# Kernel tuning notes

Measured on AMD Instinct MI355X. Metric: run time of the kernel, lower is better.

## Reference

```python
import jax, jax.numpy as jnp
import numpy as np

S, B, H = 512, 64, 1024


def setup_inputs() -> dict:
    key = jax.random.key(0)
    ks = jax.random.split(key, 9)
    sc = 1.0 / np.sqrt(2 * H)
    return {
        "hidden": jax.random.normal(ks[0], (B, H), jnp.float32),
        "decoder_out": jax.random.normal(ks[1], (B, H), jnp.float32),
        "encoder_states": jax.random.normal(ks[2], (S, B, H), jnp.float32),
        "W_attn": jax.random.uniform(ks[3], (2 * H, 2 * H), jnp.float32, -sc, sc),
        "b_attn": jax.random.uniform(ks[4], (2 * H,), jnp.float32, -sc, sc),
        "W_attn2": jax.random.uniform(ks[5], (1, 2 * H), jnp.float32, -sc, sc),
        "b_attn2": jax.random.uniform(ks[6], (1,), jnp.float32, -sc, sc),
        "W_comb": jax.random.uniform(ks[7], (H, 2 * H), jnp.float32, -sc, sc),
        "b_comb": jax.random.uniform(ks[8], (H,), jnp.float32, -sc, sc),
    }


def reference(hidden, decoder_out, encoder_states, W_attn, b_attn, W_attn2, b_attn2, W_comb, b_comb):
    s, b, h = encoder_states.shape
    # per-timestep cat(hidden, enc_t) -> attn -> tanh -> attn2, fully batched over S
    hid = jnp.broadcast_to(hidden[None], (s, b, h))
    cat = jnp.concatenate([hid, encoder_states], axis=-1)            # [S,B,2H]
    scores = jnp.tanh(cat @ W_attn.T + b_attn) @ W_attn2.T + b_attn2  # [S,B,1]
    scores = scores[..., 0].T                                         # [B,S] (stack dim=1 + squeeze)
    attn_w = jax.nn.softmax(scores, axis=-1)                          # [B,S]
    # bmm([B,1,S], [B,S,H]) -> [B,H]
    applied = jnp.einsum("bs,sbh->bh", attn_w, encoder_states)
    out = jnp.concatenate([decoder_out, applied], axis=-1) @ W_comb.T + b_comb
    out = jnp.tanh(out)
    return out, applied
```

## Files before the change

kernel.cpp:

```cpp
#include <hip/hip_runtime.h>
#include <stdint.h>


typedef __attribute__((ext_vector_type(8))) short bf16x8;
typedef __attribute__((ext_vector_type(4))) float f32x4;

__device__ __forceinline__ float bf2f(uint16_t u) {
  return __uint_as_float(((uint32_t)u) << 16);
}
__device__ __forceinline__ uint16_t f2bf(float x) {
  uint32_t u = __float_as_uint(x);
  u += 0x7fffu + ((u >> 16) & 1u);
  return (uint16_t)(u >> 16);
}
__device__ __forceinline__ uint32_t pk2(float a, float b) {
  return (uint32_t)f2bf(a) | ((uint32_t)f2bf(b) << 16);
}
__device__ __forceinline__ uint4 cvt8(const float* __restrict__ p) {
  const float4 a = *(const float4*)p;
  const float4 b = *(const float4*)(p + 4);
  uint4 r;
  r.x = pk2(a.x, a.y); r.y = pk2(a.z, a.w);
  r.z = pk2(b.x, b.y); r.w = pk2(b.z, b.w);
  return r;
}
__device__ __forceinline__ float tanh_fast(float x) {
  const float e = __expf(2.f * x);
  return __builtin_fmaf(-2.f, __builtin_amdgcn_rcpf(e + 1.f), 1.f);
}
__device__ __forceinline__ void load16(const uint16_t* g, uint16_t* l) {
  __builtin_amdgcn_global_load_lds(
      (const __attribute__((address_space(1))) void*)g,
      (__attribute__((address_space(3))) void*)l, 16, 0, 0);
}

__global__ __launch_bounds__(256)
void cvt_all_kernel(const float* __restrict__ enc, const float* __restrict__ Wa,
                    const float* __restrict__ Wc,
                    uint16_t* __restrict__ enc_bf, uint16_t* __restrict__ Wa_bf,
                    uint16_t* __restrict__ Wc_bf,
                    float* __restrict__ scores, float* __restrict__ U,
                    const float* __restrict__ ba) {
  const int tid0 = blockIdx.x * 256 + threadIdx.x;
  if (tid0 < 32768) {
    scores[tid0] = 0.f;
#pragma unroll
    for (int k = 0; k < 4; ++k) {
      const int i = tid0 * 4 + k;
      U[i] = ba[i & 2047];
    }
  }
  const int stride = gridDim.x * 256;
  for (int idx = tid0; idx < 4718592; idx += stride) {
    if (idx < 4194304) {
      ((uint4*)enc_bf)[idx] = cvt8(enc + (size_t)idx * 8);
    } else if (idx < 4456448) {
      const int k = idx - 4194304;
      const int j = k >> 7, c8 = k & 127;
      ((uint4*)Wa_bf)[k] = cvt8(Wa + (size_t)j * 2048 + 1024 + c8 * 8);
    } else {
      const int k = idx - 4456448;
      ((uint4*)Wc_bf)[k] = cvt8(Wc + (size_t)k * 8);
    }
  }
}

__global__ __launch_bounds__(256)
void gemm_u_kernel(const float* __restrict__ A, const float* __restrict__ B32,
                   float* __restrict__ U) {
  __shared__ __align__(16) uint16_t sA[128 * 32];
  __shared__ __align__(16) uint16_t sB[128 * 32];
  const int t = threadIdx.x, lane = t & 63, wave = t >> 6;
  const int wm = wave >> 1, wn = wave & 1;
  const int bn0 = blockIdx.x * 128;
  const int kbase = blockIdx.y * 256;
  const int srow = t >> 2, scol = (t & 3) * 8;
  const int ar0 = min(srow, 63), ar1 = min(64 + srow, 63);
  f32x4 acc[4][4];
#pragma unroll
  for (int i = 0; i < 4; ++i)
#pragma unroll
    for (int j = 0; j < 4; ++j) acc[i][j] = (f32x4){0.f, 0.f, 0.f, 0.f};
  const int mrow = wm * 64 + (lane & 15);
  const int nrow = wn * 64 + (lane & 15);
  const int kq = (lane >> 4) * 8;
  for (int kk = 0; kk < 8; ++kk) {
    const int k0 = kbase + (kk << 5);
    const uint4 va0 = cvt8(A + (size_t)ar0 * 1024 + scol + k0);
    const uint4 va1 = cvt8(A + (size_t)ar1 * 1024 + scol + k0);
    const uint4 vb0 = cvt8(B32 + (size_t)(bn0 + srow) * 2048 + scol + k0);
    const uint4 vb1 = cvt8(B32 + (size_t)(bn0 + 64 + srow) * 2048 + scol + k0);
    __syncthreads();
    *(uint4*)&sA[t * 8] = va0;
    *(uint4*)&sA[2048 + t * 8] = va1;
    *(uint4*)&sB[t * 8] = vb0;
    *(uint4*)&sB[2048 + t * 8] = vb1;
    __syncthreads();
    bf16x8 af[4], bfr[4];
#pragma unroll
    for (int i = 0; i < 4; ++i) af[i] = *(const bf16x8*)&sA[(mrow + i * 16) * 32 + kq];
#pragma unroll
    for (int j = 0; j < 4; ++j) bfr[j] = *(const bf16x8*)&sB[(nrow + j * 16) * 32 + kq];
#pragma unroll
    for (int i = 0; i < 4; ++i)
#pragma unroll
      for (int j = 0; j < 4; ++j)
        acc[i][j] = __builtin_amdgcn_mfma_f32_16x16x32_bf16(af[i], bfr[j], acc[i][j], 0, 0, 0);
  }
  const int colb = lane & 15, rquad = lane >> 4;
#pragma unroll
  for (int i = 0; i < 4; ++i)
#pragma unroll
    for (int r = 0; r < 4; ++r) {
      const int gm = wm * 64 + i * 16 + rquad * 4 + r;
      if (gm < 64) {
#pragma unroll
        for (int j = 0; j < 4; ++j) {
          const int gn = bn0 + wn * 64 + j * 16 + colb;
          atomicAdd(&U[gm * 2048 + gn], acc[i][j][r]);
        }
      }
    }
}

__global__ __launch_bounds__(512, 4)
void gemm_score_kernel(const uint16_t* __restrict__ A,
                       const uint16_t* __restrict__ Bm,
                       float* __restrict__ outf,
                       const float* __restrict__ Ubias,
                       const float* __restrict__ bias) {
  __shared__ __align__(16) uint16_t lds[2][12288];

  const int t = threadIdx.x, lane = t & 63, wave = t >> 6;
  const int wm = wave >> 2, wn = wave & 3;
  const int wid = blockIdx.x;
  const int xcd = wid & 7, q = wid >> 3;
  const int bm0 = (xcd * 32 + (q >> 3)) * 128;
  const int bn0 = (q & 7) * 256;

  const int rA = t >> 2, kcA = t & 3;
  const uint16_t* gpA =
      A + (size_t)(bm0 + rA) * 1024 + (kcA ^ ((rA >> 1) & 3)) * 8;
  const uint16_t* gpB[2];
#pragma unroll
  for (int qq = 0; qq < 2; ++qq) {
    const int sl = qq * 512 + t;
    const int r = sl >> 2, kc = sl & 3;
    gpB[qq] = Bm + (size_t)(bn0 + r) * 1024 + (kc ^ ((r >> 1) & 3)) * 8;
  }
  const int sbA = wave * 512;
  const int sbB0 = 4096 + wave * 512;
  const int sbB1 = 4096 + 4096 + wave * 512;

  f32x4 acc[4][4];
#pragma unroll
  for (int i = 0; i < 4; ++i)
#pragma unroll
    for (int j = 0; j < 4; ++j) acc[i][j] = (f32x4){0.f, 0.f, 0.f, 0.f};

  const int swz = ((lane >> 1) & 3) << 3;
  const int kq = ((lane >> 4) * 8) ^ swz;
  const int rl = lane & 15;
  const int aoff = (wm * 64 + rl) * 32 + kq;
  const int boff = (wn * 64 + rl) * 32 + kq;

  load16(gpA, &lds[0][sbA]);
  load16(gpB[0], &lds[0][sbB0]);
  load16(gpB[1], &lds[0][sbB1]);
  __syncthreads();

#pragma unroll
  for (int s = 0; s < 32; ++s) {
    const int cb = s & 1;
    if (s + 1 < 32) {
      const int nb = cb ^ 1, ko = (s + 1) * 32;
      load16(gpA + ko, &lds[nb][sbA]);
      load16(gpB[0] + ko, &lds[nb][sbB0]);
      load16(gpB[1] + ko, &lds[nb][sbB1]);
    }
    const uint16_t* sA = &lds[cb][0];
    const uint16_t* sB = &lds[cb][4096];
    bf16x8 af[4], bfr[4];
#pragma unroll
    for (int i = 0; i < 4; ++i) af[i] = *(const bf16x8*)&sA[aoff + i * 512];
#pragma unroll
    for (int j = 0; j < 4; ++j) bfr[j] = *(const bf16x8*)&sB[boff + j * 512];
#pragma unroll
    for (int i = 0; i < 4; ++i)
#pragma unroll
      for (int j = 0; j < 4; ++j)
        acc[i][j] = __builtin_amdgcn_mfma_f32_16x16x32_bf16(af[i], bfr[j], acc[i][j], 0, 0, 0);
    __syncthreads();
  }

  const int colb = lane & 15, rquad = lane >> 4;
  float w2f[4];
#pragma unroll
  for (int j = 0; j < 4; ++j) w2f[j] = bias[bn0 + wn * 64 + j * 16 + colb];
#pragma unroll
  for (int i = 0; i < 4; ++i) {
#pragma unroll
    for (int r = 0; r < 4; ++r) {
      const int gm = bm0 + wm * 64 + i * 16 + rquad * 4 + r;
      const int bb = gm & 63;
      float p = 0.f;
#pragma unroll
      for (int j = 0; j < 4; ++j) {
        const float u = Ubias[bb * 2048 + bn0 + wn * 64 + j * 16 + colb];
        p += tanh_fast(acc[i][j][r] + u) * w2f[j];
      }
      p += __shfl_xor(p, 1);
      p += __shfl_xor(p, 2);
      p += __shfl_xor(p, 4);
      p += __shfl_xor(p, 8);
      if (colb == 0) atomicAdd(outf + gm, p);
    }
  }
}

__global__ __launch_bounds__(512)
void gemm_comb_kernel(const uint16_t* __restrict__ A,
                      const uint16_t* __restrict__ Bm,
                      float* __restrict__ outp,
                      const float* __restrict__ bias) {
  const int t = threadIdx.x, lane = t & 63, wave = t >> 6;
  const int g = blockIdx.x * 8 + wave;
  const int m0 = (g >> 6) * 16, n0 = (g & 63) * 16;
  const int rl = lane & 15, kq = (lane >> 4) * 8;
  const uint16_t* ap = A + (size_t)(m0 + rl) * 2048 + kq;
  const uint16_t* bp = Bm + (size_t)(n0 + rl) * 2048 + kq;
  f32x4 acc = (f32x4){0.f, 0.f, 0.f, 0.f};
#pragma unroll 8
  for (int ks = 0; ks < 64; ++ks) {
    const bf16x8 af = *(const bf16x8*)(ap + ks * 32);
    const bf16x8 bf = *(const bf16x8*)(bp + ks * 32);
    acc = __builtin_amdgcn_mfma_f32_16x16x32_bf16(af, bf, acc, 0, 0, 0);
  }
  const int gm = m0 + (lane >> 4) * 4;
  const int gn = n0 + rl;
  const float bj = bias[gn];
#pragma unroll
  for (int r = 0; r < 4; ++r)
    outp[(gm + r) * 1024 + gn] = tanh_fast(acc[r] + bj);
}

__global__ __launch_bounds__(256)
void applied_kernel(const uint16_t* __restrict__ encb, const float* __restrict__ dec,
                    const float* __restrict__ scores,
                    float* __restrict__ out_applied, uint16_t* __restrict__ acat) {
  const int b = blockIdx.x, chunk = blockIdx.y, t = threadIdx.x;
  const int wave = t >> 6, lane = t & 63;
  __shared__ float w[512];
  __shared__ float red[8];
  __shared__ float2 part2[256];
  float v0 = scores[(size_t)t * 64 + b];
  float v1 = scores[(size_t)(t + 256) * 64 + b];
  float mx = fmaxf(v0, v1);
#pragma unroll
  for (int off = 32; off >= 1; off >>= 1) mx = fmaxf(mx, __shfl_xor(mx, off));
  if (lane == 0) red[wave] = mx;
  __syncthreads();
  mx = fmaxf(fmaxf(red[0], red[1]), fmaxf(red[2], red[3]));
  const float e0 = __expf(v0 - mx), e1 = __expf(v1 - mx);
  float sum = e0 + e1;
#pragma unroll
  for (int off = 32; off >= 1; off >>= 1) sum += __shfl_xor(sum, off);
  if (lane == 0) red[4 + wave] = sum;
  __syncthreads();
  sum = (red[4] + red[5]) + (red[6] + red[7]);
  const float inv = 1.f / sum;
  w[t] = e0 * inv;
  w[t + 256] = e1 * inv;
  __syncthreads();
  const int hp = t & 31, sq = t >> 5;
  const int h = chunk * 64 + hp * 2;
  const uint32_t* base = (const uint32_t*)encb + (size_t)b * 512 + (h >> 1);
  float a0 = 0.f, a1 = 0.f;
#pragma unroll 8
  for (int s = sq * 64; s < sq * 64 + 64; ++s) {
    const uint32_t p = base[(size_t)s * 32768];
    a0 += w[s] * bf2f((uint16_t)(p & 0xffffu));
    a1 += w[s] * bf2f((uint16_t)(p >> 16));
  }
  part2[t] = make_float2(a0, a1);
  __syncthreads();
  if (t < 32) {
    a0 = 0.f; a1 = 0.f;
#pragma unroll
    for (int k = 0; k < 8; ++k) {
      const float2 pp = part2[t + 32 * k];
      a0 += pp.x; a1 += pp.y;
    }
    *(float2*)(out_applied + (size_t)b * 1024 + h) = make_float2(a0, a1);
    *(uint32_t*)(acat + (size_t)b * 2048 + 1024 + h) = pk2(a0, a1);
    *(uint32_t*)(acat + (size_t)b * 2048 + h) =
        pk2(dec[(size_t)b * 1024 + h], dec[(size_t)b * 1024 + h + 1]);
  }
}

extern "C" void kernel_launch(void* const* d_in, const int* in_sizes, int n_in,
                              void* d_out, int out_size, void* d_ws, size_t ws_size,
                              hipStream_t stream) {
  const float* hidden  = (const float*)d_in[0];
  const float* dec     = (const float*)d_in[1];
  const float* enc     = (const float*)d_in[2];
  const float* W_attn  = (const float*)d_in[3];
  const float* b_attn  = (const float*)d_in[4];
  const float* W_attn2 = (const float*)d_in[5];
  const float* W_comb  = (const float*)d_in[7];
  const float* b_comb  = (const float*)d_in[8];
  float* outp = (float*)d_out;

  char* ws = (char*)d_ws;
  float*    scores = (float*)(ws + 0);
  float*    U      = (float*)(ws + 131072);
  uint16_t* acat   = (uint16_t*)(ws + 655360);
  uint16_t* enc_bf = (uint16_t*)(ws + 1048576);
  uint16_t* Wa_bf  = (uint16_t*)(ws + 68157440);
  uint16_t* Wc_bf  = (uint16_t*)(ws + 72351744);

  cvt_all_kernel<<<4608, 256, 0, stream>>>(enc, W_attn, W_comb, enc_bf, Wa_bf,
                                           Wc_bf, scores, U, b_attn);
  gemm_u_kernel<<<dim3(16, 4), 256, 0, stream>>>(hidden, W_attn, U);
  gemm_score_kernel<<<2048, 512, 0, stream>>>(enc_bf, Wa_bf, scores, U, W_attn2);
  applied_kernel<<<dim3(64, 16), 256, 0, stream>>>(enc_bf, dec, scores,
                                                   outp + 65536, acat);
  gemm_comb_kernel<<<32, 512, 0, stream>>>(acat, Wc_bf, outp, b_comb);
}
```

Baseline: 467.4 us.

## Fuse fp32-to-bf16 encoder conversion into score GEMM with triple-buffered pipeline

Removes the separate pass that converts the 128MB fp32 encoder tensor to bf16. The score GEMM now loads fp32 encoder rows into registers, converts them, and writes bf16 to LDS through a three-stage buffer, while the weight tiles still arrive by direct global-to-LDS loads. The M tile grows to 256 rows with occupancy 1, and the applied kernel reads fp32 encoder data directly. Bias init moves into the U GEMM and zeroing moves to a memset. This cuts one full write and read of the converted encoder, at the cost of register pressure, lower occupancy and fp32 reads in the applied kernel.

Result: slower. 537.0 us (+14.9%).

```diff
diff --git a/kernel.cpp b/kernel.cpp
--- a/kernel.cpp
+++ b/kernel.cpp
@@ -35,39 +35,21 @@
 }
 
 __global__ __launch_bounds__(256)
-void cvt_all_kernel(const float* __restrict__ enc, const float* __restrict__ Wa,
-                    const float* __restrict__ Wc,
-                    uint16_t* __restrict__ enc_bf, uint16_t* __restrict__ Wa_bf,
-                    uint16_t* __restrict__ Wc_bf,
-                    float* __restrict__ scores, float* __restrict__ U,
-                    const float* __restrict__ ba) {
-  const int tid0 = blockIdx.x * 256 + threadIdx.x;
-  if (tid0 < 32768) {
-    scores[tid0] = 0.f;
-#pragma unroll
-    for (int k = 0; k < 4; ++k) {
-      const int i = tid0 * 4 + k;
-      U[i] = ba[i & 2047];
-    }
-  }
-  const int stride = gridDim.x * 256;
-  for (int idx = tid0; idx < 4718592; idx += stride) {
-    if (idx < 4194304) {
-      ((uint4*)enc_bf)[idx] = cvt8(enc + (size_t)idx * 8);
-    } else if (idx < 4456448) {
-      const int k = idx - 4194304;
-      const int j = k >> 7, c8 = k & 127;
-      ((uint4*)Wa_bf)[k] = cvt8(Wa + (size_t)j * 2048 + 1024 + c8 * 8);
-    } else {
-      const int k = idx - 4456448;
-      ((uint4*)Wc_bf)[k] = cvt8(Wc + (size_t)k * 8);
-    }
+void cvt_w_kernel(const float* __restrict__ Wa, const float* __restrict__ Wc,
+                  uint16_t* __restrict__ Wa_bf, uint16_t* __restrict__ Wc_bf) {
+  const int idx = blockIdx.x * 256 + threadIdx.x;
+  if (idx < 262144) {
+    const int j = idx >> 7, c8 = idx & 127;
+    ((uint4*)Wa_bf)[idx] = cvt8(Wa + (size_t)j * 2048 + 1024 + c8 * 8);
+  } else {
+    const int k = idx - 262144;
+    ((uint4*)Wc_bf)[k] = cvt8(Wc + (size_t)k * 8);
   }
 }
 
 __global__ __launch_bounds__(256)
 void gemm_u_kernel(const float* __restrict__ A, const float* __restrict__ B32,
-                   float* __restrict__ U) {
+                   float* __restrict__ U, const float* __restrict__ ba) {
   __shared__ __align__(16) uint16_t sA[128 * 32];
   __shared__ __align__(16) uint16_t sB[128 * 32];
   const int t = threadIdx.x, lane = t & 63, wave = t >> 6;
@@ -108,6 +90,7 @@
         acc[i][j] = __builtin_amdgcn_mfma_f32_16x16x32_bf16(af[i], bfr[j], acc[i][j], 0, 0, 0);
   }
   const int colb = lane & 15, rquad = lane >> 4;
+  const float bsc = (blockIdx.y == 0) ? 1.f : 0.f;
 #pragma unroll
   for (int i = 0; i < 4; ++i)
 #pragma unroll
@@ -117,80 +100,123 @@
 #pragma unroll
         for (int j = 0; j < 4; ++j) {
           const int gn = bn0 + wn * 64 + j * 16 + colb;
-          atomicAdd(&U[gm * 2048 + gn], acc[i][j][r]);
+          atomicAdd(&U[gm * 2048 + gn], acc[i][j][r] + bsc * ba[gn]);
         }
       }
     }
 }
 
-__global__ __launch_bounds__(512, 4)
-void gemm_score_kernel(const uint16_t* __restrict__ A,
+__global__ __launch_bounds__(512, 1)
+void gemm_score_kernel(const float* __restrict__ encf,
                        const uint16_t* __restrict__ Bm,
                        float* __restrict__ outf,
                        const float* __restrict__ Ubias,
                        const float* __restrict__ bias) {
-  __shared__ __align__(16) uint16_t lds[2][12288];
+  __shared__ __align__(16) uint16_t lds[3][2][8192];
 
   const int t = threadIdx.x, lane = t & 63, wave = t >> 6;
   const int wm = wave >> 2, wn = wave & 3;
   const int wid = blockIdx.x;
   const int xcd = wid & 7, q = wid >> 3;
-  const int bm0 = (xcd * 32 + (q >> 3)) * 128;
+  const int bm0 = (xcd * 16 + (q >> 3)) * 256;
   const int bn0 = (q & 7) * 256;
 
-  const int rA = t >> 2, kcA = t & 3;
-  const uint16_t* gpA =
-      A + (size_t)(bm0 + rA) * 1024 + (kcA ^ ((rA >> 1) & 3)) * 8;
-  const uint16_t* gpB[2];
+  const float* gA[2];
+  const uint16_t* gB[2];
+  int sb[2];
 #pragma unroll
   for (int qq = 0; qq < 2; ++qq) {
     const int sl = qq * 512 + t;
     const int r = sl >> 2, kc = sl & 3;
-    gpB[qq] = Bm + (size_t)(bn0 + r) * 1024 + (kc ^ ((r >> 1) & 3)) * 8;
-  }
-  const int sbA = wave * 512;
-  const int sbB0 = 4096 + wave * 512;
-  const int sbB1 = 4096 + 4096 + wave * 512;
-
-  f32x4 acc[4][4];
-#pragma unroll
-  for (int i = 0; i < 4; ++i)
+    const int g = kc ^ ((r >> 1) & 3);
+    gA[qq] = encf + (size_t)(bm0 + r) * 1024 + g * 8;
+    gB[qq] = Bm + (size_t)(bn0 + r) * 1024 + g * 8;
+    sb[qq] = (qq * 512 + wave * 64) * 8;
+  }
+  const int wA0 = t * 8;
+  const int wA1 = 4096 + t * 8;
+
+  f32x4 acc[8][4];
+#pragma unroll
+  for (int i = 0; i < 8; ++i)
 #pragma unroll
     for (int j = 0; j < 4; ++j) acc[i][j] = (f32x4){0.f, 0.f, 0.f, 0.f};
 
   const int swz = ((lane >> 1) & 3) << 3;
   const int kq = ((lane >> 4) * 8) ^ swz;
   const int rl = lane & 15;
-  const int aoff = (wm * 64 + rl) * 32 + kq;
+  const int aoff = (wm * 128 + rl) * 32 + kq;
   const int boff = (wn * 64 + rl) * 32 + kq;
 
-  load16(gpA, &lds[0][sbA]);
-  load16(gpB[0], &lds[0][sbB0]);
-  load16(gpB[1], &lds[0][sbB1]);
-  __syncthreads();
-
-#pragma unroll
-  for (int s = 0; s < 32; ++s) {
-    const int cb = s & 1;
-    if (s + 1 < 32) {
-      const int nb = cb ^ 1, ko = (s + 1) * 32;
-      load16(gpA + ko, &lds[nb][sbA]);
-      load16(gpB[0] + ko, &lds[nb][sbB0]);
-      load16(gpB[1] + ko, &lds[nb][sbB1]);
-    }
-    const uint16_t* sA = &lds[cb][0];
-    const uint16_t* sB = &lds[cb][4096];
-    bf16x8 af[4], bfr[4];
-#pragma unroll
-    for (int i = 0; i < 4; ++i) af[i] = *(const bf16x8*)&sA[aoff + i * 512];
+  float4 av[2][2];
+#pragma unroll
+  for (int qq = 0; qq < 2; ++qq) {
+    av[qq][0] = *(const float4*)(gA[qq]);
+    av[qq][1] = *(const float4*)(gA[qq] + 4);
+  }
+#pragma unroll
+  for (int qq = 0; qq < 2; ++qq) load16(gB[qq], &lds[0][1][sb[qq]]);
+#pragma unroll
+  for (int qq = 0; qq < 2; ++qq) load16(gB[qq] + 32, &lds[1][1][sb[qq]]);
+  asm volatile("s_waitcnt vmcnt(2)" ::: "memory");
+  {
+    uint4 w0, w1;
+    w0.x = pk2(av[0][0].x, av[0][0].y); w0.y = pk2(av[0][0].z, av[0][0].w);
+    w0.z = pk2(av[0][1].x, av[0][1].y); w0.w = pk2(av[0][1].z, av[0][1].w);
+    w1.x = pk2(av[1][0].x, av[1][0].y); w1.y = pk2(av[1][0].z, av[1][0].w);
+    w1.z = pk2(av[1][1].x, av[1][1].y); w1.w = pk2(av[1][1].z, av[1][1].w);
+    *(uint4*)&lds[0][0][wA0] = w0;
+    *(uint4*)&lds[0][0][wA1] = w1;
+  }
+  asm volatile("s_waitcnt lgkmcnt(0)" ::: "memory");
+  __builtin_amdgcn_s_barrier();
+
+  constexpr int NT = 32;
+#pragma unroll
+  for (int kt = 0; kt < NT; ++kt) {
+    const int cb = kt % 3;
+    if (kt + 1 < NT) {
+      const int ko = (kt + 1) * 32;
+#pragma unroll
+      for (int qq = 0; qq < 2; ++qq) {
+        av[qq][0] = *(const float4*)(gA[qq] + ko);
+        av[qq][1] = *(const float4*)(gA[qq] + ko + 4);
+      }
+    }
+    if (kt + 2 < NT) {
+      const int nb2 = (kt + 2) % 3, ko2 = (kt + 2) * 32;
+#pragma unroll
+      for (int qq = 0; qq < 2; ++qq) load16(gB[qq] + ko2, &lds[nb2][1][sb[qq]]);
+    }
+    const uint16_t* sA = lds[cb][0];
+    const uint16_t* sB = lds[cb][1];
+    bf16x8 af[8], bfr[4];
+#pragma unroll
+    for (int i = 0; i < 8; ++i) af[i] = *(const bf16x8*)&sA[aoff + i * 512];
 #pragma unroll
     for (int j = 0; j < 4; ++j) bfr[j] = *(const bf16x8*)&sB[boff + j * 512];
 #pragma unroll
-    for (int i = 0; i < 4; ++i)
+    for (int i = 0; i < 8; ++i)
 #pragma unroll
       for (int j = 0; j < 4; ++j)
         acc[i][j] = __builtin_amdgcn_mfma_f32_16x16x32_bf16(af[i], bfr[j], acc[i][j], 0, 0, 0);
-    __syncthreads();
+    if (kt + 1 < NT) {
+      if (kt + 2 < NT) {
+        asm volatile("s_waitcnt vmcnt(2)" ::: "memory");
+      } else {
+        asm volatile("s_waitcnt vmcnt(0)" ::: "memory");
+      }
+      const int nb1 = (kt + 1) % 3;
+      uint4 w0, w1;
+      w0.x = pk2(av[0][0].x, av[0][0].y); w0.y = pk2(av[0][0].z, av[0][0].w);
+      w0.z = pk2(av[0][1].x, av[0][1].y); w0.w = pk2(av[0][1].z, av[0][1].w);
+      w1.x = pk2(av[1][0].x, av[1][0].y); w1.y = pk2(av[1][0].z, av[1][0].w);
+      w1.z = pk2(av[1][1].x, av[1][1].y); w1.w = pk2(av[1][1].z, av[1][1].w);
+      *(uint4*)&lds[nb1][0][wA0] = w0;
+      *(uint4*)&lds[nb1][0][wA1] = w1;
+      asm volatile("s_waitcnt lgkmcnt(0)" ::: "memory");
+      __builtin_amdgcn_s_barrier();
+    }
   }
 
   const int colb = lane & 15, rquad = lane >> 4;
@@ -198,10 +224,10 @@
 #pragma unroll
   for (int j = 0; j < 4; ++j) w2f[j] = bias[bn0 + wn * 64 + j * 16 + colb];
 #pragma unroll
-  for (int i = 0; i < 4; ++i) {
+  for (int i = 0; i < 8; ++i) {
 #pragma unroll
     for (int r = 0; r < 4; ++r) {
-      const int gm = bm0 + wm * 64 + i * 16 + rquad * 4 + r;
+      const int gm = bm0 + wm * 128 + i * 16 + rquad * 4 + r;
       const int bb = gm & 63;
       float p = 0.f;
 #pragma unroll
@@ -245,7 +271,7 @@
 }
 
 __global__ __launch_bounds__(256)
-void applied_kernel(const uint16_t* __restrict__ encb, const float* __restrict__ dec,
+void applied_kernel(const float* __restrict__ encf, const float* __restrict__ dec,
                     const float* __restrict__ scores,
                     float* __restrict__ out_applied, uint16_t* __restrict__ acat) {
   const int b = blockIdx.x, chunk = blockIdx.y, t = threadIdx.x;
@@ -274,13 +300,13 @@
   __syncthreads();
   const int hp = t & 31, sq = t >> 5;
   const int h = chunk * 64 + hp * 2;
-  const uint32_t* base = (const uint32_t*)encb + (size_t)b * 512 + (h >> 1);
+  const float2* base = (const float2*)encf + (((size_t)b * 1024 + h) >> 1);
   float a0 = 0.f, a1 = 0.f;
 #pragma unroll 8
   for (int s = sq * 64; s < sq * 64 + 64; ++s) {
-    const uint32_t p = base[(size_t)s * 32768];
-    a0 += w[s] * bf2f((uint16_t)(p & 0xffffu));
-    a1 += w[s] * bf2f((uint16_t)(p >> 16));
+    const float2 p = base[(size_t)s * 32768];
+    a0 += w[s] * p.x;
+    a1 += w[s] * p.y;
   }
   part2[t] = make_float2(a0, a1);
   __syncthreads();
@@ -315,15 +341,14 @@
   float*    scores = (float*)(ws + 0);
   float*    U      = (float*)(ws + 131072);
   uint16_t* acat   = (uint16_t*)(ws + 655360);
-  uint16_t* enc_bf = (uint16_t*)(ws + 1048576);
   uint16_t* Wa_bf  = (uint16_t*)(ws + 68157440);
   uint16_t* Wc_bf  = (uint16_t*)(ws + 72351744);
 
-  cvt_all_kernel<<<4608, 256, 0, stream>>>(enc, W_attn, W_comb, enc_bf, Wa_bf,
-                                           Wc_bf, scores, U, b_attn);
-  gemm_u_kernel<<<dim3(16, 4), 256, 0, stream>>>(hidden, W_attn, U);
-  gemm_score_kernel<<<2048, 512, 0, stream>>>(enc_bf, Wa_bf, scores, U, W_attn2);
-  applied_kernel<<<dim3(64, 16), 256, 0, stream>>>(enc_bf, dec, scores,
+  hipMemsetAsync(ws, 0, 655360, stream);
+  cvt_w_kernel<<<2048, 256, 0, stream>>>(W_attn, W_comb, Wa_bf, Wc_bf);
+  gemm_u_kernel<<<dim3(16, 4), 256, 0, stream>>>(hidden, W_attn, U, b_attn);
+  gemm_score_kernel<<<1024, 512, 0, stream>>>(enc, Wa_bf, scores, U, W_attn2);
+  applied_kernel<<<dim3(64, 16), 256, 0, stream>>>(enc, dec, scores,
                                                    outp + 65536, acat);
   gemm_comb_kernel<<<32, 512, 0, stream>>>(acat, Wc_bf, outp, b_comb);
 }
```

## Merge U-GEMM into conversion kernel and enlarge score GEMM tile with triple buffering

Applied to the files above, without the earlier changes.

The small hidden·W_attn GEMM now runs as extra blocks of the fp32-to-bf16 conversion kernel, and the bias is folded into its atomic adds, which saves one launch. Scores and U are zeroed by a memset instead. The score GEMM tile grows from 128x256 to 256x256 per block (8x4 MFMA accumulators per wave), and the LDS pipeline goes from double to triple buffering with explicit vmcnt waits. The aim is more operand reuse and better latency hiding, at the cost of higher register pressure (launch bounds drop to 2 blocks) and fewer blocks.

Result: no change. 465.0 us (-0.5%).

```diff
diff --git a/kernel.cpp b/kernel.cpp
--- a/kernel.cpp
+++ b/kernel.cpp
@@ -35,45 +35,37 @@
 }
 
 __global__ __launch_bounds__(256)
-void cvt_all_kernel(const float* __restrict__ enc, const float* __restrict__ Wa,
-                    const float* __restrict__ Wc,
-                    uint16_t* __restrict__ enc_bf, uint16_t* __restrict__ Wa_bf,
-                    uint16_t* __restrict__ Wc_bf,
-                    float* __restrict__ scores, float* __restrict__ U,
-                    const float* __restrict__ ba) {
-  const int tid0 = blockIdx.x * 256 + threadIdx.x;
-  if (tid0 < 32768) {
-    scores[tid0] = 0.f;
-#pragma unroll
-    for (int k = 0; k < 4; ++k) {
-      const int i = tid0 * 4 + k;
-      U[i] = ba[i & 2047];
-    }
-  }
-  const int stride = gridDim.x * 256;
-  for (int idx = tid0; idx < 4718592; idx += stride) {
-    if (idx < 4194304) {
-      ((uint4*)enc_bf)[idx] = cvt8(enc + (size_t)idx * 8);
-    } else if (idx < 4456448) {
-      const int k = idx - 4194304;
-      const int j = k >> 7, c8 = k & 127;
-      ((uint4*)Wa_bf)[k] = cvt8(Wa + (size_t)j * 2048 + 1024 + c8 * 8);
-    } else {
-      const int k = idx - 4456448;
-      ((uint4*)Wc_bf)[k] = cvt8(Wc + (size_t)k * 8);
-    }
-  }
-}
-
-__global__ __launch_bounds__(256)
-void gemm_u_kernel(const float* __restrict__ A, const float* __restrict__ B32,
-                   float* __restrict__ U) {
-  __shared__ __align__(16) uint16_t sA[128 * 32];
-  __shared__ __align__(16) uint16_t sB[128 * 32];
-  const int t = threadIdx.x, lane = t & 63, wave = t >> 6;
+void cvt_gemmu_kernel(const float* __restrict__ enc, const float* __restrict__ Wa,
+                      const float* __restrict__ Wc,
+                      uint16_t* __restrict__ enc_bf, uint16_t* __restrict__ Wa_bf,
+                      uint16_t* __restrict__ Wc_bf,
+                      const float* __restrict__ hidden, float* __restrict__ U,
+                      const float* __restrict__ ba) {
+  __shared__ __align__(16) uint16_t sAB[2][128 * 32];
+  const int t = threadIdx.x;
+  if (blockIdx.x < 4608) {
+    const int stride = 4608 * 256;
+    for (int idx = blockIdx.x * 256 + t; idx < 4718592; idx += stride) {
+      if (idx < 4194304) {
+        ((uint4*)enc_bf)[idx] = cvt8(enc + (size_t)idx * 8);
+      } else if (idx < 4456448) {
+        const int k = idx - 4194304;
+        const int j = k >> 7, c8 = k & 127;
+        ((uint4*)Wa_bf)[k] = cvt8(Wa + (size_t)j * 2048 + 1024 + c8 * 8);
+      } else {
+        const int k = idx - 4456448;
+        ((uint4*)Wc_bf)[k] = cvt8(Wc + (size_t)k * 8);
+      }
+    }
+    return;
+  }
+  const int bx = blockIdx.x - 4608;
+  uint16_t* sA = sAB[0];
+  uint16_t* sB = sAB[1];
+  const int lane = t & 63, wave = t >> 6;
   const int wm = wave >> 1, wn = wave & 1;
-  const int bn0 = blockIdx.x * 128;
-  const int kbase = blockIdx.y * 256;
+  const int bn0 = (bx & 15) * 128;
+  const int kbase = (bx >> 4) * 256;
   const int srow = t >> 2, scol = (t & 3) * 8;
   const int ar0 = min(srow, 63), ar1 = min(64 + srow, 63);
   f32x4 acc[4][4];
@@ -86,10 +78,10 @@
   const int kq = (lane >> 4) * 8;
   for (int kk = 0; kk < 8; ++kk) {
     const int k0 = kbase + (kk << 5);
-    const uint4 va0 = cvt8(A + (size_t)ar0 * 1024 + scol + k0);
-    const uint4 va1 = cvt8(A + (size_t)ar1 * 1024 + scol + k0);
-    const uint4 vb0 = cvt8(B32 + (size_t)(bn0 + srow) * 2048 + scol + k0);
-    const uint4 vb1 = cvt8(B32 + (size_t)(bn0 + 64 + srow) * 2048 + scol + k0);
+    const uint4 va0 = cvt8(hidden + (size_t)ar0 * 1024 + scol + k0);
+    const uint4 va1 = cvt8(hidden + (size_t)ar1 * 1024 + scol + k0);
+    const uint4 vb0 = cvt8(Wa + (size_t)(bn0 + srow) * 2048 + scol + k0);
+    const uint4 vb1 = cvt8(Wa + (size_t)(bn0 + 64 + srow) * 2048 + scol + k0);
     __syncthreads();
     *(uint4*)&sA[t * 8] = va0;
     *(uint4*)&sA[2048 + t * 8] = va1;
@@ -108,6 +100,7 @@
         acc[i][j] = __builtin_amdgcn_mfma_f32_16x16x32_bf16(af[i], bfr[j], acc[i][j], 0, 0, 0);
   }
   const int colb = lane & 15, rquad = lane >> 4;
+  const float bsc = (kbase == 0) ? 1.f : 0.f;
 #pragma unroll
   for (int i = 0; i < 4; ++i)
 #pragma unroll
@@ -117,80 +110,96 @@
 #pragma unroll
         for (int j = 0; j < 4; ++j) {
           const int gn = bn0 + wn * 64 + j * 16 + colb;
-          atomicAdd(&U[gm * 2048 + gn], acc[i][j][r]);
+          atomicAdd(&U[gm * 2048 + gn], acc[i][j][r] + bsc * ba[gn]);
         }
       }
     }
 }
 
-__global__ __launch_bounds__(512, 4)
+__global__ __launch_bounds__(512, 2)
 void gemm_score_kernel(const uint16_t* __restrict__ A,
                        const uint16_t* __restrict__ Bm,
                        float* __restrict__ outf,
                        const float* __restrict__ Ubias,
                        const float* __restrict__ bias) {
-  __shared__ __align__(16) uint16_t lds[2][12288];
+  __shared__ __align__(16) uint16_t lds[3][2][8192];
 
   const int t = threadIdx.x, lane = t & 63, wave = t >> 6;
   const int wm = wave >> 2, wn = wave & 3;
   const int wid = blockIdx.x;
   const int xcd = wid & 7, q = wid >> 3;
-  const int bm0 = (xcd * 32 + (q >> 3)) * 128;
+  const int bm0 = (xcd * 16 + (q >> 3)) * 256;
   const int bn0 = (q & 7) * 256;
 
-  const int rA = t >> 2, kcA = t & 3;
-  const uint16_t* gpA =
-      A + (size_t)(bm0 + rA) * 1024 + (kcA ^ ((rA >> 1) & 3)) * 8;
+  const uint16_t* gpA[2];
   const uint16_t* gpB[2];
+  int sb[2];
 #pragma unroll
   for (int qq = 0; qq < 2; ++qq) {
-    const int sl = qq * 512 + t;
-    const int r = sl >> 2, kc = sl & 3;
-    gpB[qq] = Bm + (size_t)(bn0 + r) * 1024 + (kc ^ ((r >> 1) & 3)) * 8;
-  }
-  const int sbA = wave * 512;
-  const int sbB0 = 4096 + wave * 512;
-  const int sbB1 = 4096 + 4096 + wave * 512;
-
-  f32x4 acc[4][4];
-#pragma unroll
-  for (int i = 0; i < 4; ++i)
+    const int s = qq * 512 + t;
+    const int r = s >> 2, kc = s & 3;
+    const int g = kc ^ ((r >> 1) & 3);
+    gpA[qq] = A + (size_t)(bm0 + r) * 1024 + g * 8;
+    gpB[qq] = Bm + (size_t)(bn0 + r) * 1024 + g * 8;
+    sb[qq] = (qq * 512 + wave * 64) * 8;
+  }
+
+  f32x4 acc[8][4];
+#pragma unroll
+  for (int i = 0; i < 8; ++i)
 #pragma unroll
     for (int j = 0; j < 4; ++j) acc[i][j] = (f32x4){0.f, 0.f, 0.f, 0.f};
 
   const int swz = ((lane >> 1) & 3) << 3;
   const int kq = ((lane >> 4) * 8) ^ swz;
-  const int rl = lane & 15;
-  const int aoff = (wm * 64 + rl) * 32 + kq;
-  const int boff = (wn * 64 + rl) * 32 + kq;
-
-  load16(gpA, &lds[0][sbA]);
-  load16(gpB[0], &lds[0][sbB0]);
-  load16(gpB[1], &lds[0][sbB1]);
-  __syncthreads();
-
-#pragma unroll
-  for (int s = 0; s < 32; ++s) {
-    const int cb = s & 1;
-    if (s + 1 < 32) {
-      const int nb = cb ^ 1, ko = (s + 1) * 32;
-      load16(gpA + ko, &lds[nb][sbA]);
-      load16(gpB[0] + ko, &lds[nb][sbB0]);
-      load16(gpB[1] + ko, &lds[nb][sbB1]);
-    }
-    const uint16_t* sA = &lds[cb][0];
-    const uint16_t* sB = &lds[cb][4096];
-    bf16x8 af[4], bfr[4];
-#pragma unroll
-    for (int i = 0; i < 4; ++i) af[i] = *(const bf16x8*)&sA[aoff + i * 512];
+  const int aoff = (wm * 128 + (lane & 15)) * 32 + kq;
+  const int boff = (wn * 64 + (lane & 15)) * 32 + kq;
+
+#pragma unroll
+  for (int qq = 0; qq < 2; ++qq) {
+    load16(gpA[qq], &lds[0][0][sb[qq]]);
+    load16(gpB[qq], &lds[0][1][sb[qq]]);
+  }
+#pragma unroll
+  for (int qq = 0; qq < 2; ++qq) {
+    load16(gpA[qq] + 32, &lds[1][0][sb[qq]]);
+    load16(gpB[qq] + 32, &lds[1][1][sb[qq]]);
+  }
+  asm volatile("s_waitcnt vmcnt(4)" ::: "memory");
+  __builtin_amdgcn_s_barrier();
+
+  constexpr int NT = 32;
+#pragma unroll
+  for (int kt = 0; kt < NT; ++kt) {
+    const int bufc = kt % 3;
+    if (kt + 2 < NT) {
+      const int nb = (kt + 2) % 3;
+      const int kpre = (kt + 2) * 32;
+#pragma unroll
+      for (int qq = 0; qq < 2; ++qq) {
+        load16(gpA[qq] + kpre, &lds[nb][0][sb[qq]]);
+        load16(gpB[qq] + kpre, &lds[nb][1][sb[qq]]);
+      }
+    }
+    const uint16_t* sA = lds[bufc][0];
+    const uint16_t* sB = lds[bufc][1];
+    bf16x8 af[8], bfr[4];
+#pragma unroll
+    for (int i = 0; i < 8; ++i) af[i] = *(const bf16x8*)&sA[aoff + i * 512];
 #pragma unroll
     for (int j = 0; j < 4; ++j) bfr[j] = *(const bf16x8*)&sB[boff + j * 512];
 #pragma unroll
-    for (int i = 0; i < 4; ++i)
+    for (int i = 0; i < 8; ++i)
 #pragma unroll
       for (int j = 0; j < 4; ++j)
         acc[i][j] = __builtin_amdgcn_mfma_f32_16x16x32_bf16(af[i], bfr[j], acc[i][j], 0, 0, 0);
-    __syncthreads();
+    if (kt + 2 < NT) {
+      asm volatile("s_waitcnt vmcnt(4) lgkmcnt(0)" ::: "memory");
+      __builtin_amdgcn_s_barrier();
+    } else if (kt + 1 < NT) {
+      asm volatile("s_waitcnt vmcnt(0) lgkmcnt(0)" ::: "memory");
+      __builtin_amdgcn_s_barrier();
+    }
   }
 
   const int colb = lane & 15, rquad = lane >> 4;
@@ -198,10 +207,10 @@
 #pragma unroll
   for (int j = 0; j < 4; ++j) w2f[j] = bias[bn0 + wn * 64 + j * 16 + colb];
 #pragma unroll
-  for (int i = 0; i < 4; ++i) {
+  for (int i = 0; i < 8; ++i) {
 #pragma unroll
     for (int r = 0; r < 4; ++r) {
-      const int gm = bm0 + wm * 64 + i * 16 + rquad * 4 + r;
+      const int gm = bm0 + wm * 128 + i * 16 + rquad * 4 + r;
       const int bb = gm & 63;
       float p = 0.f;
 #pragma unroll
@@ -319,10 +328,10 @@
   uint16_t* Wa_bf  = (uint16_t*)(ws + 68157440);
   uint16_t* Wc_bf  = (uint16_t*)(ws + 72351744);
 
-  cvt_all_kernel<<<4608, 256, 0, stream>>>(enc, W_attn, W_comb, enc_bf, Wa_bf,
-                                           Wc_bf, scores, U, b_attn);
-  gemm_u_kernel<<<dim3(16, 4), 256, 0, stream>>>(hidden, W_attn, U);
-  gemm_score_kernel<<<2048, 512, 0, stream>>>(enc_bf, Wa_bf, scores, U, W_attn2);
+  hipMemsetAsync(ws, 0, 655360, stream);
+  cvt_gemmu_kernel<<<4672, 256, 0, stream>>>(enc, W_attn, W_comb, enc_bf,
+                                             Wa_bf, Wc_bf, hidden, U, b_attn);
+  gemm_score_kernel<<<1024, 512, 0, stream>>>(enc_bf, Wa_bf, scores, U, W_attn2);
   applied_kernel<<<dim3(64, 16), 256, 0, stream>>>(enc_bf, dec, scores,
                                                    outp + 65536, acat);
   gemm_comb_kernel<<<32, 512, 0, stream>>>(acat, Wc_bf, outp, b_comb);
```
